# Performance work log

Hardware: AMD Instinct MI355X
Metric: run time of the kernel (lower is better)

Reference implementation:

```python
import jax, jax.numpy as jnp
import numpy as np

N_NODES = 32768
N_EDGES = 524288
N_FEAT = 256
HID = 256
N_GRAPHS = 64
N_CLASSES = 4
NODES_PER_GRAPH = N_NODES // N_GRAPHS
BN_EPS = 1e-5


def setup_inputs() -> dict:
    key = jax.random.key(0)
    ks = jax.random.split(key, 16)
    x = jax.random.normal(ks[0], (N_NODES, N_FEAT), dtype=jnp.float32)
    edge_index = jax.random.randint(ks[1], (2, N_EDGES), 0, N_NODES, dtype=jnp.int32)
    batch = (jnp.arange(N_NODES, dtype=jnp.int32) // NODES_PER_GRAPH)
    def xavier(k, shape):
        fan_in, fan_out = shape[0], shape[1]
        a = float(np.sqrt(6.0 / (fan_in + fan_out)))
        return jax.random.uniform(k, shape, jnp.float32, -a, a)
    return {
        "x": x, "edge_index": edge_index, "batch": batch,
        "W1": xavier(ks[2], (N_FEAT, HID)), "b1": jnp.zeros((HID,), jnp.float32),
        "g1": jnp.ones((HID,), jnp.float32), "be1": jnp.zeros((HID,), jnp.float32),
        "W2": xavier(ks[3], (HID, HID)), "b2": jnp.zeros((HID,), jnp.float32),
        "g2": jnp.ones((HID,), jnp.float32), "be2": jnp.zeros((HID,), jnp.float32),
        "W_ih": xavier(ks[4], (HID, 4 * HID)), "W_hh": xavier(ks[5], (HID, 4 * HID)),
        "b_ih": jnp.zeros((4 * HID,), jnp.float32), "b_hh": jnp.zeros((4 * HID,), jnp.float32),
        "W_fc": xavier(ks[6], (HID, N_CLASSES)), "b_fc": jnp.zeros((N_CLASSES,), jnp.float32),
    }


def gcn_conv(x, W, b, src, dst):
    # PyG GCNConv: add self-loops, symmetric normalization, aggregate, then bias
    h = x @ W                                   # [N, H]
    deg = jnp.zeros((x.shape[0],), h.dtype).at[dst].add(1.0) + 1.0  # in-deg + self-loop
    dinv = jax.lax.rsqrt(deg)
    coef = dinv[src] * dinv[dst]                # [E]
    msg = h[src] * coef[:, None]                # gather + scale, [E, H]
    agg = jnp.zeros_like(h).at[dst].add(msg)    # scatter-add
    agg = agg + h * (1.0 / deg)[:, None]        # self-loop term (norm = 1/deg)
    return agg + b


def batch_norm(x, gamma, beta):
    mean = jnp.mean(x, axis=0)
    var = jnp.mean(jnp.square(x - mean), axis=0)  # biased, as torch BN training
    return (x - mean) * jax.lax.rsqrt(var + BN_EPS) * gamma + beta


def reference(x, edge_index, batch, W1, b1, g1, be1, W2, b2, g2, be2,
              W_ih, W_hh, b_ih, b_hh, W_fc, b_fc):
    src, dst = edge_index[0], edge_index[1]
    h = jax.nn.relu(batch_norm(gcn_conv(x, W1, b1, src, dst), g1, be1))
    h = jax.nn.relu(batch_norm(gcn_conv(h, W2, b2, src, dst), g2, be2))
    # global mean pool over graphs
    sums = jax.ops.segment_sum(h, batch, num_segments=N_GRAPHS)
    cnts = jax.ops.segment_sum(jnp.ones((h.shape[0],), h.dtype), batch, num_segments=N_GRAPHS)
    pooled = sums / cnts[:, None]               # [G, H]
    # LSTM, seq_len = 1, zero initial state -> single cell step
    h0 = jnp.zeros((N_GRAPHS, HID), h.dtype)
    c0 = jnp.zeros((N_GRAPHS, HID), h.dtype)
    gates = pooled @ W_ih + h0 @ W_hh + b_ih + b_hh  # [G, 4H]
    i, f, g, o = jnp.split(gates, 4, axis=1)
    c1 = jax.nn.sigmoid(f) * c0 + jax.nn.sigmoid(i) * jnp.tanh(g)
    h1 = jax.nn.sigmoid(o) * jnp.tanh(c1)
    logits = h1 @ W_fc + b_fc
    logp = jax.nn.log_softmax(logits, axis=1)
    return (logp, (h1[None], c1[None]))
```

## Files before the change

kernel.cpp:

```cpp
#include <hip/hip_runtime.h>
#include <math.h>

#define N_NODES 32768
#define N_FEAT 256
#define HID 256
#define N_GRAPHS 64
#define NPG 512
#define N_CLASSES 4
#define BN_EPS 1e-5f

typedef __attribute__((ext_vector_type(8))) short bf16x8;
typedef __attribute__((ext_vector_type(4))) float f32x4;

__device__ __forceinline__ ushort f2b(float f) {
    union { float f; uint u; } v; v.f = f;
    uint u = v.u;
    return (ushort)((u + 0x7FFFu + ((u >> 16) & 1u)) >> 16);
}
__device__ __forceinline__ float bflo(uint u) {
    union { uint u; float f; } v; v.u = u << 16;
    return v.f;
}
__device__ __forceinline__ float bfhi(uint u) {
    union { uint u; float f; } v; v.u = u & 0xFFFF0000u;
    return v.f;
}

__global__ void k_count_prep(const int* __restrict__ dst, int* __restrict__ degcnt, int cntB,
                             const float* __restrict__ W1, const float* __restrict__ W2,
                             ushort* __restrict__ Wt1, ushort* __restrict__ Wt2, int E) {
    int b = blockIdx.x;
    int t = threadIdx.x;
    if (b < cntB) {
        int e = b * 256 + t;
        if (e < E) atomicAdd(&degcnt[dst[e]], 1);
    } else {
        int wb = b - cntB;
        const float* W = (wb < 256) ? W1 : W2;
        ushort* Wt = (wb < 256) ? Wt1 : Wt2;
        int n = wb & 255;
        Wt[n * 256 + t] = f2b(W[t * 256 + n]);
    }
}

__global__ __launch_bounds__(256) void k_scan1(const int* __restrict__ degcnt,
                                               int* __restrict__ blocksum,
                                               ushort* __restrict__ hs_pad) {
    int n = blockIdx.x * 256 + threadIdx.x;
    int p = (degcnt[n] + 2) & ~1;
#pragma unroll
    for (int off = 1; off < 64; off <<= 1) p += __shfl_xor(p, off);
    __shared__ int ws[4];
    int lane = threadIdx.x & 63, w = threadIdx.x >> 6;
    if (lane == 0) ws[w] = p;
    __syncthreads();
    if (threadIdx.x == 0)
        blocksum[blockIdx.x] = ws[0] + ws[1] + ws[2] + ws[3];
    if (blockIdx.x == 0 && threadIdx.x < 128)
        ((uint*)hs_pad)[threadIdx.x] = 0;
}

__global__ __launch_bounds__(256) void k_scan3(const int* __restrict__ degcnt,
                                               const int* __restrict__ blocksum,
                                               float* __restrict__ dinv,
                                               int* __restrict__ row_start,
                                               int* __restrict__ cursor,
                                               uint* __restrict__ csrs) {
    __shared__ int bs[128];
    __shared__ int ws[4];
    int t = threadIdx.x;
    if (t < 128) bs[t] = blocksum[t];
    int n = blockIdx.x * 256 + t;
    int c = degcnt[n];
    int p = (c + 2) & ~1;
    int lane = t & 63, w = t >> 6;
    int inc = p;
#pragma unroll
    for (int off = 1; off < 64; off <<= 1) {
        int u = __shfl_up(inc, off);
        if (lane >= off) inc += u;
    }
    if (lane == 63) ws[w] = inc;
    __syncthreads();
    int boff = 0;
    for (int i = 0; i < blockIdx.x; ++i) boff += bs[i];
    int wadd = 0;
    for (int i = 0; i < w; ++i) wadd += ws[i];
    int run = boff + wadd + inc - p;
    row_start[n] = run;
    csrs[run] = (uint)n;
    if (!(c & 1)) csrs[run + c + 1] = N_NODES;
    cursor[n] = run + 1;
    dinv[n] = rsqrtf((float)(c + 1));
    if (blockIdx.x == 127 && t == 255) row_start[N_NODES] = run + p;
}

__global__ void k_fill(const int* __restrict__ src, const int* __restrict__ dst,
                       int* __restrict__ cursor, uint* __restrict__ csrs, int E) {
    int e = blockIdx.x * 256 + threadIdx.x;
    if (e >= E) return;
    int d = dst[e];
    int pos = atomicAdd(&cursor[d], 1);
    csrs[pos] = (uint)src[e];
}

template <int MODE>
__device__ __forceinline__ void gemm_body(const ushort* __restrict__ A,
                                          const float* __restrict__ Af,
                                          const ushort* __restrict__ Bt,
                                          const float* __restrict__ dinv,
                                          const float* __restrict__ bnsum,
                                          const float* __restrict__ bnsq,
                                          const float* __restrict__ gamma,
                                          const float* __restrict__ beta,
                                          ushort* __restrict__ hs) {
    __shared__ ushort Bs[128 * 256];
    __shared__ float2 bnc[256];
    int tid = threadIdx.x;
    int n0 = blockIdx.x * 128;
    int m0 = blockIdx.y * 128;

    if (MODE == 1) {
        const float invN = 1.0f / (float)N_NODES;
        float mean = bnsum[tid] * invN;
        float var = bnsq[tid] * invN - mean * mean;
        float sc = rsqrtf(var + BN_EPS) * gamma[tid];
        bnc[tid] = make_float2(sc, beta[tid] - mean * sc);
    }

#pragma unroll
    for (int c = 0; c < 16; ++c) {
        int g = c * 256 + tid;
        int idx = g * 8;
        int row = idx >> 8;
        int col = idx & 255;
        uint4 v = *(const uint4*)(Bt + (size_t)(n0 + row) * 256 + col);
        int sidx = idx ^ ((row & 7) << 3);
        *(uint4*)(Bs + sidx) = v;
    }
    __syncthreads();

    int wid = tid >> 6;
    int lane = tid & 63;
    int wr = wid >> 1, wc = wid & 1;
    int r = lane & 15;
    int ko = (lane >> 4) * 8;

    const ushort* Ab = (MODE != 2) ? A + (size_t)(m0 + wr * 64 + r) * 256 + ko : nullptr;
    const float*  Afb = (MODE == 2) ? Af + (size_t)(m0 + wr * 64 + r) * 256 + ko : nullptr;

    f32x4 acc[4][4] = {};
#pragma unroll
    for (int ks = 0; ks < 8; ++ks) {
        bf16x8 a[4], b[4];
        if (MODE == 1) {
            int kb = ko + ks * 32;
            float2 c0 = bnc[kb + 0], c1 = bnc[kb + 1], c2 = bnc[kb + 2], c3 = bnc[kb + 3];
            float2 c4 = bnc[kb + 4], c5 = bnc[kb + 5], c6 = bnc[kb + 6], c7 = bnc[kb + 7];
#pragma unroll
            for (int i = 0; i < 4; ++i) {
                uint4 v = *(const uint4*)(Ab + i * (16 * 256) + ks * 32);
                float f0 = fmaxf(bflo(v.x) * c0.x + c0.y, 0.f);
                float f1 = fmaxf(bfhi(v.x) * c1.x + c1.y, 0.f);
                float f2 = fmaxf(bflo(v.y) * c2.x + c2.y, 0.f);
                float f3 = fmaxf(bfhi(v.y) * c3.x + c3.y, 0.f);
                float f4 = fmaxf(bflo(v.z) * c4.x + c4.y, 0.f);
                float f5 = fmaxf(bfhi(v.z) * c5.x + c5.y, 0.f);
                float f6 = fmaxf(bflo(v.w) * c6.x + c6.y, 0.f);
                float f7 = fmaxf(bfhi(v.w) * c7.x + c7.y, 0.f);
                uint4 o;
                o.x = (uint)f2b(f0) | ((uint)f2b(f1) << 16);
                o.y = (uint)f2b(f2) | ((uint)f2b(f3) << 16);
                o.z = (uint)f2b(f4) | ((uint)f2b(f5) << 16);
                o.w = (uint)f2b(f6) | ((uint)f2b(f7) << 16);
                a[i] = *(bf16x8*)&o;
            }
        } else if (MODE == 2) {
#pragma unroll
            for (int i = 0; i < 4; ++i) {
                float4 v0 = *(const float4*)(Afb + i * (16 * 256) + ks * 32);
                float4 v1 = *(const float4*)(Afb + i * (16 * 256) + ks * 32 + 4);
                uint4 o;
                o.x = (uint)f2b(v0.x) | ((uint)f2b(v0.y) << 16);
                o.y = (uint)f2b(v0.z) | ((uint)f2b(v0.w) << 16);
                o.z = (uint)f2b(v1.x) | ((uint)f2b(v1.y) << 16);
                o.w = (uint)f2b(v1.z) | ((uint)f2b(v1.w) << 16);
                a[i] = *(bf16x8*)&o;
            }
        } else {
#pragma unroll
            for (int i = 0; i < 4; ++i)
                a[i] = *(const bf16x8*)(Ab + i * (16 * 256) + ks * 32);
        }
#pragma unroll
        for (int j = 0; j < 4; ++j) {
            int srow = wc * 64 + j * 16 + r;
            int idx = (srow * 256 + ko + ks * 32) ^ ((srow & 7) << 3);
            b[j] = *(const bf16x8*)(Bs + idx);
        }
#pragma unroll
        for (int i = 0; i < 4; ++i)
#pragma unroll
            for (int j = 0; j < 4; ++j)
                acc[i][j] = __builtin_amdgcn_mfma_f32_16x16x32_bf16(a[i], b[j], acc[i][j], 0, 0, 0);
    }

    int rr = (lane >> 4) * 4;
    int cc = lane & 15;
#pragma unroll
    for (int i = 0; i < 4; ++i) {
        int row = m0 + wr * 64 + i * 16 + rr;
#pragma unroll
        for (int r2 = 0; r2 < 4; ++r2) {
            float dv = dinv[row + r2];
#pragma unroll
            for (int j = 0; j < 4; ++j) {
                int col = n0 + wc * 64 + j * 16 + cc;
                hs[(size_t)(row + r2) * 256 + col] = f2b(acc[i][j][r2] * dv);
            }
        }
    }
}

__global__ __launch_bounds__(256) void k_gemm_cvt(const float* __restrict__ Af,
                                                  const ushort* __restrict__ Bt,
                                                  const float* __restrict__ dinv,
                                                  ushort* __restrict__ hs) {
    gemm_body<2>(nullptr, Af, Bt, dinv, nullptr, nullptr, nullptr, nullptr, hs);
}

__global__ __launch_bounds__(256) void k_gemm_bn(const ushort* __restrict__ A,
                                                 const ushort* __restrict__ Bt,
                                                 const float* __restrict__ dinv,
                                                 const float* __restrict__ bnsum,
                                                 const float* __restrict__ bnsq,
                                                 const float* __restrict__ gamma,
                                                 const float* __restrict__ beta,
                                                 ushort* __restrict__ hs) {
    gemm_body<1>(A, nullptr, Bt, dinv, bnsum, bnsq, gamma, beta, hs);
}

__global__ __launch_bounds__(256) void k_agg(const ushort* __restrict__ hs,
                                             const uint* __restrict__ csrs,
                                             const int* __restrict__ row_start,
                                             const float* __restrict__ dinv,
                                             const float* __restrict__ bias,
                                             ushort* __restrict__ aggb) {
    int wid = threadIdx.x >> 6;
    int lane = threadIdx.x & 63;
    int half = lane >> 5;
    int fq = lane & 31;
    int n = blockIdx.x * 4 + wid;

    float dv = dinv[n];
    int base = row_start[n];
    int pairs = (row_start[n + 1] - base) >> 1;

    float a0 = 0.f, a1 = 0.f, a2 = 0.f, a3 = 0.f, a4 = 0.f, a5 = 0.f, a6 = 0.f, a7 = 0.f;

    int t = 0;
    for (; t + 8 <= pairs; t += 8) {
        uint s0 = csrs[base + 2 * t + 0 + half];
        uint s1 = csrs[base + 2 * t + 2 + half];
        uint s2 = csrs[base + 2 * t + 4 + half];
        uint s3 = csrs[base + 2 * t + 6 + half];
        uint s4 = csrs[base + 2 * t + 8 + half];
        uint s5 = csrs[base + 2 * t + 10 + half];
        uint s6 = csrs[base + 2 * t + 12 + half];
        uint s7 = csrs[base + 2 * t + 14 + half];
        uint4 h0 = *(const uint4*)(hs + (size_t)s0 * 256 + fq * 8);
        uint4 h1 = *(const uint4*)(hs + (size_t)s1 * 256 + fq * 8);
        uint4 h2 = *(const uint4*)(hs + (size_t)s2 * 256 + fq * 8);
        uint4 h3 = *(const uint4*)(hs + (size_t)s3 * 256 + fq * 8);
        uint4 h4 = *(const uint4*)(hs + (size_t)s4 * 256 + fq * 8);
        uint4 h5 = *(const uint4*)(hs + (size_t)s5 * 256 + fq * 8);
        uint4 h6 = *(const uint4*)(hs + (size_t)s6 * 256 + fq * 8);
        uint4 h7 = *(const uint4*)(hs + (size_t)s7 * 256 + fq * 8);
        a0 += bflo(h0.x) + bflo(h1.x) + bflo(h2.x) + bflo(h3.x)
            + bflo(h4.x) + bflo(h5.x) + bflo(h6.x) + bflo(h7.x);
        a1 += bfhi(h0.x) + bfhi(h1.x) + bfhi(h2.x) + bfhi(h3.x)
            + bfhi(h4.x) + bfhi(h5.x) + bfhi(h6.x) + bfhi(h7.x);
        a2 += bflo(h0.y) + bflo(h1.y) + bflo(h2.y) + bflo(h3.y)
            + bflo(h4.y) + bflo(h5.y) + bflo(h6.y) + bflo(h7.y);
        a3 += bfhi(h0.y) + bfhi(h1.y) + bfhi(h2.y) + bfhi(h3.y)
            + bfhi(h4.y) + bfhi(h5.y) + bfhi(h6.y) + bfhi(h7.y);
        a4 += bflo(h0.z) + bflo(h1.z) + bflo(h2.z) + bflo(h3.z)
            + bflo(h4.z) + bflo(h5.z) + bflo(h6.z) + bflo(h7.z);
        a5 += bfhi(h0.z) + bfhi(h1.z) + bfhi(h2.z) + bfhi(h3.z)
            + bfhi(h4.z) + bfhi(h5.z) + bfhi(h6.z) + bfhi(h7.z);
        a6 += bflo(h0.w) + bflo(h1.w) + bflo(h2.w) + bflo(h3.w)
            + bflo(h4.w) + bflo(h5.w) + bflo(h6.w) + bflo(h7.w);
        a7 += bfhi(h0.w) + bfhi(h1.w) + bfhi(h2.w) + bfhi(h3.w)
            + bfhi(h4.w) + bfhi(h5.w) + bfhi(h6.w) + bfhi(h7.w);
    }
    for (; t + 2 <= pairs; t += 2) {
        uint s0 = csrs[base + 2 * t + 0 + half];
        uint s1 = csrs[base + 2 * t + 2 + half];
        uint4 h0 = *(const uint4*)(hs + (size_t)s0 * 256 + fq * 8);
        uint4 h1 = *(const uint4*)(hs + (size_t)s1 * 256 + fq * 8);
        a0 += bflo(h0.x) + bflo(h1.x);
        a1 += bfhi(h0.x) + bfhi(h1.x);
        a2 += bflo(h0.y) + bflo(h1.y);
        a3 += bfhi(h0.y) + bfhi(h1.y);
        a4 += bflo(h0.z) + bflo(h1.z);
        a5 += bfhi(h0.z) + bfhi(h1.z);
        a6 += bflo(h0.w) + bflo(h1.w);
        a7 += bfhi(h0.w) + bfhi(h1.w);
    }
    if (t < pairs) {
        uint s0 = csrs[base + 2 * t + half];
        uint4 h0 = *(const uint4*)(hs + (size_t)s0 * 256 + fq * 8);
        a0 += bflo(h0.x); a1 += bfhi(h0.x);
        a2 += bflo(h0.y); a3 += bfhi(h0.y);
        a4 += bflo(h0.z); a5 += bfhi(h0.z);
        a6 += bflo(h0.w); a7 += bfhi(h0.w);
    }

    a0 += __shfl_xor(a0, 32); a1 += __shfl_xor(a1, 32);
    a2 += __shfl_xor(a2, 32); a3 += __shfl_xor(a3, 32);
    a4 += __shfl_xor(a4, 32); a5 += __shfl_xor(a5, 32);
    a6 += __shfl_xor(a6, 32); a7 += __shfl_xor(a7, 32);

    if (half == 0) {
        float4 b0 = *(const float4*)&bias[fq * 8];
        float4 b1 = *(const float4*)&bias[fq * 8 + 4];
        float o0 = a0 * dv + b0.x, o1 = a1 * dv + b0.y;
        float o2 = a2 * dv + b0.z, o3 = a3 * dv + b0.w;
        float o4 = a4 * dv + b1.x, o5 = a5 * dv + b1.y;
        float o6 = a6 * dv + b1.z, o7 = a7 * dv + b1.w;
        uint4 ov;
        ov.x = (uint)f2b(o0) | ((uint)f2b(o1) << 16);
        ov.y = (uint)f2b(o2) | ((uint)f2b(o3) << 16);
        ov.z = (uint)f2b(o4) | ((uint)f2b(o5) << 16);
        ov.w = (uint)f2b(o6) | ((uint)f2b(o7) << 16);
        *(uint4*)(aggb + (size_t)n * HID + fq * 8) = ov;
    }
}

__global__ __launch_bounds__(256) void k_bn_stats(const ushort* __restrict__ aggb,
                                                  float* __restrict__ bnsum,
                                                  float* __restrict__ bnsq) {
    int t = threadIdx.x;
    int fq = t & 31;
    int rg = t >> 5;
    int r0 = blockIdx.x * 128 + rg * 16;

    float s[8] = {}, q[8] = {};
    for (int r = 0; r < 16; ++r) {
        uint4 v = *(const uint4*)(aggb + (size_t)(r0 + r) * HID + fq * 8);
        float f0 = bflo(v.x), f1 = bfhi(v.x), f2 = bflo(v.y), f3 = bfhi(v.y);
        float f4 = bflo(v.z), f5 = bfhi(v.z), f6 = bflo(v.w), f7 = bfhi(v.w);
        s[0] += f0; q[0] += f0 * f0;  s[1] += f1; q[1] += f1 * f1;
        s[2] += f2; q[2] += f2 * f2;  s[3] += f3; q[3] += f3 * f3;
        s[4] += f4; q[4] += f4 * f4;  s[5] += f5; q[5] += f5 * f5;
        s[6] += f6; q[6] += f6 * f6;  s[7] += f7; q[7] += f7 * f7;
    }

    __shared__ float red[8][32][16];
#pragma unroll
    for (int i = 0; i < 8; ++i) {
        red[rg][fq][i] = s[i];
        red[rg][fq][8 + i] = q[i];
    }
    __syncthreads();
    int fq2 = t & 31;
    int vg = t >> 5;
#pragma unroll
    for (int k = 0; k < 2; ++k) {
        int v = vg * 2 + k;
        float acc = 0.f;
#pragma unroll
        for (int rgi = 0; rgi < 8; ++rgi) acc += red[rgi][fq2][v];
        float* dstp = (v < 8) ? bnsum : bnsq;
        atomicAdd(&dstp[fq2 * 8 + (v & 7)], acc);
    }
}

__global__ __launch_bounds__(256) void k_bn_pool(const ushort* __restrict__ aggb,
                                                 const float* __restrict__ bnsum,
                                                 const float* __restrict__ bnsq,
                                                 const float* __restrict__ gamma,
                                                 const float* __restrict__ beta,
                                                 float* __restrict__ pooled) {
    int g = blockIdx.x >> 4;
    int blk = blockIdx.x & 15;
    int f = threadIdx.x;
    const float invN = 1.0f / (float)N_NODES;
    float mean = bnsum[f] * invN;
    float var = bnsq[f] * invN - mean * mean;
    float sc = rsqrtf(var + BN_EPS) * gamma[f];
    float sh = beta[f] - mean * sc;
    int r0 = g * NPG + blk * 32;
    float s = 0.0f;
#pragma unroll 4
    for (int r = 0; r < 32; ++r) {
        float v = bflo((uint)aggb[(size_t)(r0 + r) * HID + f]) * sc + sh;
        s += v > 0.0f ? v : 0.0f;
    }
    atomicAdd(&pooled[g * HID + f], s);
}

__global__ __launch_bounds__(256) void k_head(const float* __restrict__ pooled,
                                              const float* __restrict__ W_ih,
                                              const float* __restrict__ b_ih,
                                              const float* __restrict__ b_hh,
                                              const float* __restrict__ W_fc,
                                              const float* __restrict__ b_fc,
                                              float* __restrict__ out) {
    __shared__ float p[HID];
    __shared__ float lsum[N_CLASSES][256];
    __shared__ float logits[N_CLASSES];
    int g = blockIdx.x, j = threadIdx.x;
    p[j] = pooled[g * HID + j] * (1.0f / (float)NPG);
    __syncthreads();

    float gi = 0.f, gf = 0.f, gg = 0.f, go = 0.f;
#pragma unroll 4
    for (int k = 0; k < HID; ++k) {
        float pk = p[k];
        const float* w = &W_ih[(size_t)k * (4 * HID) + j];
        gi += pk * w[0];
        gf += pk * w[HID];
        gg += pk * w[2 * HID];
        go += pk * w[3 * HID];
    }
    gi += b_ih[j] + b_hh[j];
    gf += b_ih[HID + j] + b_hh[HID + j];
    gg += b_ih[2 * HID + j] + b_hh[2 * HID + j];
    go += b_ih[3 * HID + j] + b_hh[3 * HID + j];
    (void)gf;

    float si = 1.f / (1.f + expf(-gi));
    float so = 1.f / (1.f + expf(-go));
    float c1 = si * tanhf(gg);
    float h1 = so * tanhf(c1);

    out[N_GRAPHS * N_CLASSES + g * HID + j] = h1;
    out[N_GRAPHS * N_CLASSES + N_GRAPHS * HID + g * HID + j] = c1;

#pragma unroll
    for (int c = 0; c < N_CLASSES; ++c)
        lsum[c][j] = h1 * W_fc[j * N_CLASSES + c];
    __syncthreads();
    for (int s = 128; s > 0; s >>= 1) {
        if (j < s) {
#pragma unroll
            for (int c = 0; c < N_CLASSES; ++c)
                lsum[c][j] += lsum[c][j + s];
        }
        __syncthreads();
    }
    if (j < N_CLASSES) logits[j] = lsum[j][0] + b_fc[j];
    __syncthreads();
    if (j < N_CLASSES) {
        float m = fmaxf(fmaxf(logits[0], logits[1]), fmaxf(logits[2], logits[3]));
        float lse = m + logf(expf(logits[0] - m) + expf(logits[1] - m) +
                             expf(logits[2] - m) + expf(logits[3] - m));
        out[g * N_CLASSES + j] = logits[j] - lse;
    }
}

extern "C" void kernel_launch(void* const* d_in, const int* in_sizes, int n_in,
                              void* d_out, int out_size, void* d_ws, size_t ws_size,
                              hipStream_t stream) {
    const float* x    = (const float*)d_in[0];
    const int*   ei   = (const int*)d_in[1];
    const float* W1   = (const float*)d_in[3];
    const float* b1   = (const float*)d_in[4];
    const float* g1   = (const float*)d_in[5];
    const float* be1  = (const float*)d_in[6];
    const float* W2   = (const float*)d_in[7];
    const float* b2   = (const float*)d_in[8];
    const float* g2   = (const float*)d_in[9];
    const float* be2  = (const float*)d_in[10];
    const float* W_ih = (const float*)d_in[11];
    const float* b_ih = (const float*)d_in[13];
    const float* b_hh = (const float*)d_in[14];
    const float* W_fc = (const float*)d_in[15];
    const float* b_fc = (const float*)d_in[16];
    float* out = (float*)d_out;

    int E = in_sizes[1] / 2;
    const int* src = ei;
    const int* dst = ei + E;

    const size_t MAT = (size_t)N_NODES * HID;
    size_t SZ = ((size_t)E + 2 * N_NODES + 1023) & ~(size_t)1023;

    ushort* aggb = (ushort*)d_ws;
    ushort* hs   = aggb + MAT;
    ushort* Wt1  = hs + MAT + 256;
    ushort* Wt2  = Wt1 + 65536;
    float*  dinv = (float*)(Wt2 + 65536);
    int*    row_start = (int*)(dinv + N_NODES);
    int*    cursor    = row_start + N_NODES + 2;
    uint*   csrs      = (uint*)(cursor + N_NODES);
    int*    blocksum  = (int*)(csrs + SZ);
    int*    degcnt = blocksum + 128;
    float*  bn1sum = (float*)(degcnt + N_NODES);
    float*  bn1sq  = bn1sum + HID;
    float*  bn2sum = bn1sq + HID;
    float*  bn2sq  = bn2sum + HID;
    float*  pooled = bn2sq + HID;
    size_t zeroBytes = (size_t)N_NODES * 4 + 4 * HID * 4 + (size_t)N_GRAPHS * HID * 4;

    dim3 blk(256);
    int edgeBlocks = (E + 255) / 256;
    int aggBlocks = N_NODES / 4;
    dim3 gemmGrid(2, N_NODES / 128);

    hipMemsetAsync(degcnt, 0, zeroBytes, stream);

    k_count_prep<<<edgeBlocks + 512, blk, 0, stream>>>(dst, degcnt, edgeBlocks,
                                                       W1, W2, Wt1, Wt2, E);
    k_scan1<<<N_NODES / 256, blk, 0, stream>>>(degcnt, blocksum, hs + MAT);
    k_scan3<<<N_NODES / 256, blk, 0, stream>>>(degcnt, blocksum, dinv, row_start, cursor, csrs);
    k_fill<<<edgeBlocks, blk, 0, stream>>>(src, dst, cursor, csrs, E);

    k_gemm_cvt<<<gemmGrid, blk, 0, stream>>>(x, Wt1, dinv, hs);
    k_agg<<<aggBlocks, blk, 0, stream>>>(hs, csrs, row_start, dinv, b1, aggb);
    k_bn_stats<<<N_NODES / 128, blk, 0, stream>>>(aggb, bn1sum, bn1sq);

    k_gemm_bn<<<gemmGrid, blk, 0, stream>>>(aggb, Wt2, dinv, bn1sum, bn1sq, g1, be1, hs);
    k_agg<<<aggBlocks, blk, 0, stream>>>(hs, csrs, row_start, dinv, b2, aggb);
    k_bn_stats<<<N_NODES / 128, blk, 0, stream>>>(aggb, bn2sum, bn2sq);

    k_bn_pool<<<N_GRAPHS * 16, blk, 0, stream>>>(aggb, bn2sum, bn2sq, g2, be2, pooled);
    k_head<<<N_GRAPHS, blk, 0, stream>>>(pooled, W_ih, b_ih, b_hh, W_fc, b_fc, out);
}
```

Before: 280.9 us.

## Fuse BN statistics into aggregation kernel with slotted atomic partial sums

Removes the separate batch-norm statistics kernel by having each aggregation block reduce the sum and sum of squares of its four output rows in shared memory and atomically add them into one of 64 slot buffers. Consumers (the second GEMM and the pooling kernel) then sum the 64 slots per feature. This avoids re-reading the bf16 aggregation output twice and saves two launches. In exchange it adds a __syncthreads and 512 atomics per aggregation block (8192 blocks), spread across slots to limit contention.

```diff
diff --git a/kernel.cpp b/kernel.cpp
--- a/kernel.cpp
+++ b/kernel.cpp
@@ -8,6 +8,7 @@
 #define NPG 512
 #define N_CLASSES 4
 #define BN_EPS 1e-5f
+#define NSLOT 64
 
 typedef __attribute__((ext_vector_type(8))) short bf16x8;
 typedef __attribute__((ext_vector_type(4))) float f32x4;
@@ -109,8 +110,7 @@
                                           const float* __restrict__ Af,
                                           const ushort* __restrict__ Bt,
                                           const float* __restrict__ dinv,
-                                          const float* __restrict__ bnsum,
-                                          const float* __restrict__ bnsq,
+                                          const float* __restrict__ pstat,
                                           const float* __restrict__ gamma,
                                           const float* __restrict__ beta,
                                           ushort* __restrict__ hs) {
@@ -121,9 +121,15 @@
     int m0 = blockIdx.y * 128;
 
     if (MODE == 1) {
+        float s = 0.f, q = 0.f;
+#pragma unroll 8
+        for (int i = 0; i < NSLOT; ++i) {
+            s += pstat[i * 512 + tid];
+            q += pstat[i * 512 + 256 + tid];
+        }
         const float invN = 1.0f / (float)N_NODES;
-        float mean = bnsum[tid] * invN;
-        float var = bnsq[tid] * invN - mean * mean;
+        float mean = s * invN;
+        float var = q * invN - mean * mean;
         float sc = rsqrtf(var + BN_EPS) * gamma[tid];
         bnc[tid] = make_float2(sc, beta[tid] - mean * sc);
     }
@@ -226,18 +232,17 @@
                                                   const ushort* __restrict__ Bt,
                                                   const float* __restrict__ dinv,
                                                   ushort* __restrict__ hs) {
-    gemm_body<2>(nullptr, Af, Bt, dinv, nullptr, nullptr, nullptr, nullptr, hs);
+    gemm_body<2>(nullptr, Af, Bt, dinv, nullptr, nullptr, nullptr, hs);
 }
 
 __global__ __launch_bounds__(256) void k_gemm_bn(const ushort* __restrict__ A,
                                                  const ushort* __restrict__ Bt,
                                                  const float* __restrict__ dinv,
-                                                 const float* __restrict__ bnsum,
-                                                 const float* __restrict__ bnsq,
+                                                 const float* __restrict__ pstat,
                                                  const float* __restrict__ gamma,
                                                  const float* __restrict__ beta,
                                                  ushort* __restrict__ hs) {
-    gemm_body<1>(A, nullptr, Bt, dinv, bnsum, bnsq, gamma, beta, hs);
+    gemm_body<1>(A, nullptr, Bt, dinv, pstat, gamma, beta, hs);
 }
 
 __global__ __launch_bounds__(256) void k_agg(const ushort* __restrict__ hs,
@@ -245,7 +250,8 @@
                                              const int* __restrict__ row_start,
                                              const float* __restrict__ dinv,
                                              const float* __restrict__ bias,
-                                             ushort* __restrict__ aggb) {
+                                             ushort* __restrict__ aggb,
+                                             float* __restrict__ pstat) {
     int wid = threadIdx.x >> 6;
     int lane = threadIdx.x & 63;
     int half = lane >> 5;
@@ -321,6 +327,7 @@
     a4 += __shfl_xor(a4, 32); a5 += __shfl_xor(a5, 32);
     a6 += __shfl_xor(a6, 32); a7 += __shfl_xor(a7, 32);
 
+    __shared__ float ls[4][32][16];
     if (half == 0) {
         float4 b0 = *(const float4*)&bias[fq * 8];
         float4 b1 = *(const float4*)&bias[fq * 8 + 4];
@@ -334,60 +341,47 @@
         ov.z = (uint)f2b(o4) | ((uint)f2b(o5) << 16);
         ov.w = (uint)f2b(o6) | ((uint)f2b(o7) << 16);
         *(uint4*)(aggb + (size_t)n * HID + fq * 8) = ov;
-    }
-}
-
-__global__ __launch_bounds__(256) void k_bn_stats(const ushort* __restrict__ aggb,
-                                                  float* __restrict__ bnsum,
-                                                  float* __restrict__ bnsq) {
-    int t = threadIdx.x;
-    int fq = t & 31;
-    int rg = t >> 5;
-    int r0 = blockIdx.x * 128 + rg * 16;
-
-    float s[8] = {}, q[8] = {};
-    for (int r = 0; r < 16; ++r) {
-        uint4 v = *(const uint4*)(aggb + (size_t)(r0 + r) * HID + fq * 8);
-        float f0 = bflo(v.x), f1 = bfhi(v.x), f2 = bflo(v.y), f3 = bfhi(v.y);
-        float f4 = bflo(v.z), f5 = bfhi(v.z), f6 = bflo(v.w), f7 = bfhi(v.w);
-        s[0] += f0; q[0] += f0 * f0;  s[1] += f1; q[1] += f1 * f1;
-        s[2] += f2; q[2] += f2 * f2;  s[3] += f3; q[3] += f3 * f3;
-        s[4] += f4; q[4] += f4 * f4;  s[5] += f5; q[5] += f5 * f5;
-        s[6] += f6; q[6] += f6 * f6;  s[7] += f7; q[7] += f7 * f7;
-    }
-
-    __shared__ float red[8][32][16];
-#pragma unroll
-    for (int i = 0; i < 8; ++i) {
-        red[rg][fq][i] = s[i];
-        red[rg][fq][8 + i] = q[i];
-    }
-    __syncthreads();
-    int fq2 = t & 31;
-    int vg = t >> 5;
+        float t0 = bflo(ov.x), t1 = bfhi(ov.x), t2 = bflo(ov.y), t3 = bfhi(ov.y);
+        float t4 = bflo(ov.z), t5 = bfhi(ov.z), t6 = bflo(ov.w), t7 = bfhi(ov.w);
+        ls[wid][fq][0] = t0; ls[wid][fq][1] = t1;
+        ls[wid][fq][2] = t2; ls[wid][fq][3] = t3;
+        ls[wid][fq][4] = t4; ls[wid][fq][5] = t5;
+        ls[wid][fq][6] = t6; ls[wid][fq][7] = t7;
+        ls[wid][fq][8]  = t0 * t0; ls[wid][fq][9]  = t1 * t1;
+        ls[wid][fq][10] = t2 * t2; ls[wid][fq][11] = t3 * t3;
+        ls[wid][fq][12] = t4 * t4; ls[wid][fq][13] = t5 * t5;
+        ls[wid][fq][14] = t6 * t6; ls[wid][fq][15] = t7 * t7;
+    }
+    __syncthreads();
+    int tt = threadIdx.x;
+    int fq2 = tt & 31, vg = tt >> 5;
+    float* slot = pstat + (size_t)(blockIdx.x & (NSLOT - 1)) * 512;
 #pragma unroll
     for (int k = 0; k < 2; ++k) {
         int v = vg * 2 + k;
-        float acc = 0.f;
-#pragma unroll
-        for (int rgi = 0; rgi < 8; ++rgi) acc += red[rgi][fq2][v];
-        float* dstp = (v < 8) ? bnsum : bnsq;
-        atomicAdd(&dstp[fq2 * 8 + (v & 7)], acc);
+        float acc = ls[0][fq2][v] + ls[1][fq2][v] + ls[2][fq2][v] + ls[3][fq2][v];
+        int feat = fq2 * 8 + (v & 7);
+        atomicAdd(&slot[(v < 8 ? 0 : 256) + feat], acc);
     }
 }
 
 __global__ __launch_bounds__(256) void k_bn_pool(const ushort* __restrict__ aggb,
-                                                 const float* __restrict__ bnsum,
-                                                 const float* __restrict__ bnsq,
+                                                 const float* __restrict__ pstat,
                                                  const float* __restrict__ gamma,
                                                  const float* __restrict__ beta,
                                                  float* __restrict__ pooled) {
     int g = blockIdx.x >> 4;
     int blk = blockIdx.x & 15;
     int f = threadIdx.x;
+    float su = 0.f, q = 0.f;
+#pragma unroll 8
+    for (int i = 0; i < NSLOT; ++i) {
+        su += pstat[i * 512 + f];
+        q  += pstat[i * 512 + 256 + f];
+    }
     const float invN = 1.0f / (float)N_NODES;
-    float mean = bnsum[f] * invN;
-    float var = bnsq[f] * invN - mean * mean;
+    float mean = su * invN;
+    float var = q * invN - mean * mean;
     float sc = rsqrtf(var + BN_EPS) * gamma[f];
     float sh = beta[f] - mean * sc;
     int r0 = g * NPG + blk * 32;
@@ -497,12 +491,10 @@
     uint*   csrs      = (uint*)(cursor + N_NODES);
     int*    blocksum  = (int*)(csrs + SZ);
     int*    degcnt = blocksum + 128;
-    float*  bn1sum = (float*)(degcnt + N_NODES);
-    float*  bn1sq  = bn1sum + HID;
-    float*  bn2sum = bn1sq + HID;
-    float*  bn2sq  = bn2sum + HID;
-    float*  pooled = bn2sq + HID;
-    size_t zeroBytes = (size_t)N_NODES * 4 + 4 * HID * 4 + (size_t)N_GRAPHS * HID * 4;
+    float*  pb1    = (float*)(degcnt + N_NODES);
+    float*  pb2    = pb1 + NSLOT * 512;
+    float*  pooled = pb2 + NSLOT * 512;
+    size_t zeroBytes = (size_t)N_NODES * 4 + 2 * NSLOT * 512 * 4 + (size_t)N_GRAPHS * HID * 4;
 
     dim3 blk(256);
     int edgeBlocks = (E + 255) / 256;
@@ -518,13 +510,11 @@
     k_fill<<<edgeBlocks, blk, 0, stream>>>(src, dst, cursor, csrs, E);
 
     k_gemm_cvt<<<gemmGrid, blk, 0, stream>>>(x, Wt1, dinv, hs);
-    k_agg<<<aggBlocks, blk, 0, stream>>>(hs, csrs, row_start, dinv, b1, aggb);
-    k_bn_stats<<<N_NODES / 128, blk, 0, stream>>>(aggb, bn1sum, bn1sq);
-
-    k_gemm_bn<<<gemmGrid, blk, 0, stream>>>(aggb, Wt2, dinv, bn1sum, bn1sq, g1, be1, hs);
-    k_agg<<<aggBlocks, blk, 0, stream>>>(hs, csrs, row_start, dinv, b2, aggb);
-    k_bn_stats<<<N_NODES / 128, blk, 0, stream>>>(aggb, bn2sum, bn2sq);
-
-    k_bn_pool<<<N_GRAPHS * 16, blk, 0, stream>>>(aggb, bn2sum, bn2sq, g2, be2, pooled);
+    k_agg<<<aggBlocks, blk, 0, stream>>>(hs, csrs, row_start, dinv, b1, aggb, pb1);
+
+    k_gemm_bn<<<gemmGrid, blk, 0, stream>>>(aggb, Wt2, dinv, pb1, g1, be1, hs);
+    k_agg<<<aggBlocks, blk, 0, stream>>>(hs, csrs, row_start, dinv, b2, aggb, pb2);
+
+    k_bn_pool<<<N_GRAPHS * 16, blk, 0, stream>>>(aggb, pb2, g2, be2, pooled);
     k_head<<<N_GRAPHS, blk, 0, stream>>>(pooled, W_ih, b_ih, b_hh, W_fc, b_fc, out);
 }
```

Result: slower. 315.8 us (+12.4%).
